# Optimization experiments

Measured on AMD Instinct MI355X. Metric: run time of the kernel, lower is better.

## Reference

```python
import jax, jax.numpy as jnp
import numpy as np

B, N, F_IN, F_OUT, H = 4, 2048, 256, 256, 4
NEG_INF = -1e9
EDGE_PROB = 0.05
LEAKY_SLOPE = 0.2  # tf.nn.leaky_relu default alpha


def setup_inputs() -> dict:
    key = jax.random.key(0)
    k_x, k_m, k_w, k_a, k_b = jax.random.split(key, 5)
    inputs = jax.random.normal(k_x, (B, N, F_IN), dtype=jnp.float32)
    # bias: additive adjacency mask, 0 on edges / -1e9 off-edges (standard GAT)
    u = jax.random.uniform(k_m, (B, N, N), dtype=jnp.float32)
    bias = jnp.where(u < EDGE_PROB, 0.0, NEG_INF).astype(jnp.float32)
    # self-loops so every softmax row has at least one valid entry
    bias = bias.at[:, jnp.arange(N), jnp.arange(N)].set(0.0)
    # per-head learned params (uniform [0,1) init as in the original)
    W = jax.random.uniform(k_w, (H, F_IN, F_OUT), dtype=jnp.float32)
    a = jax.random.uniform(k_a, (H, F_OUT), dtype=jnp.float32)
    b = jax.random.uniform(k_b, (H, F_OUT), dtype=jnp.float32)
    return {"inputs": inputs, "bias": bias, "W": W, "a": a, "b": b}


def reference(inputs, bias, W, a, b):
    # transformed: [H, B, N, F_OUT]
    t = jnp.einsum('bnf,hfo->hbno', inputs, W) + b[:, None, None, :]
    # per-node score s = t @ a : [H, B, N]
    s = jnp.einsum('hbno,ho->hbn', t, a)
    # weights[i,j] = s[i] + s[j]  (weights + transpose)
    w = s[..., :, None] + s[..., None, :]  # [H, B, N, N]
    coefs = jax.nn.softmax(jax.nn.leaky_relu(w, negative_slope=LEAKY_SLOPE) + bias, axis=-1)
    heads = jnp.einsum('hbnm,hbmo->hbno', coefs, t)  # [H, B, N, F_OUT]
    return jnp.mean(heads, axis=0)  # (1/num_heads) * add_n(heads)
```

## Files before the change

kernel.cpp:

```cpp
#include <hip/hip_runtime.h>
#include <hip/hip_bf16.h>
#include <stdint.h>

#define H 4
#define BB 4
#define NN 2048
#define FIN 256
#define FOUT 256
#define M_TOT (BB*NN)
#define LOG2E 1.44269504f

typedef float f32x4 __attribute__((ext_vector_type(4)));
typedef short s16x8 __attribute__((ext_vector_type(8)));
typedef unsigned int u32;

static __device__ __forceinline__ short f2bf(float f) {
    return __builtin_bit_cast(short, __float2bfloat16(f));
}
static __device__ __forceinline__ float bf2f(short u) {
    unsigned x = ((unsigned)(unsigned short)u) << 16;
    return __builtin_bit_cast(float, x);
}
static __device__ __forceinline__ void glds16(const void* g, void* l) {
    __builtin_amdgcn_global_load_lds(
        (const __attribute__((address_space(1))) u32*)(g),
        (__attribute__((address_space(3))) u32*)(l), 16, 0, 0);
}

__global__ __launch_bounds__(256) void k_prep(const float* __restrict__ W, const float* __restrict__ a,
                                              const float* __restrict__ bvec,
                                              short* __restrict__ WT, float* __restrict__ q,
                                              float* __restrict__ c) {
    int bid = blockIdx.x;
    if (bid < 64) {
        __shared__ float lds[64][65];
        int h = bid >> 4, kt = (bid >> 2) & 3, ot = bid & 3;
        int kb = kt * 64, ob = ot * 64;
        int tx = threadIdx.x & 63, ty = threadIdx.x >> 6;
#pragma unroll
        for (int r = 0; r < 16; ++r) {
            int k_l = ty + r * 4;
            lds[tx][k_l] = W[(size_t)(h * FIN + kb + k_l) * FOUT + ob + tx];
        }
        __syncthreads();
#pragma unroll
        for (int r = 0; r < 16; ++r) {
            int o_l = ty + r * 4;
            WT[(size_t)(h * FOUT + ob + o_l) * FIN + kb + tx] = f2bf(lds[o_l][tx]);
        }
    } else if (bid < 320) {
        int wv = ((bid - 64) * 256 + threadIdx.x) >> 6;
        int lane = threadIdx.x & 63;
        int h = wv >> 8, f = wv & 255;
        float4 w4 = *(const float4*)(W + (size_t)(h * FIN + f) * FOUT + lane * 4);
        float4 a4 = *(const float4*)(a + h * FOUT + lane * 4);
        float d = w4.x * a4.x + w4.y * a4.y + w4.z * a4.z + w4.w * a4.w;
#pragma unroll
        for (int off = 32; off; off >>= 1) d += __shfl_xor(d, off);
        if (lane == 0) q[h * FIN + f] = d;
    } else {
        int h = threadIdx.x >> 6, lane = threadIdx.x & 63;
        float4 b4 = *(const float4*)(bvec + h * FOUT + lane * 4);
        float4 a4 = *(const float4*)(a + h * FOUT + lane * 4);
        float d = b4.x * a4.x + b4.y * a4.y + b4.z * a4.z + b4.w * a4.w;
#pragma unroll
        for (int off = 32; off; off >>= 1) d += __shfl_xor(d, off);
        if (lane == 0) c[h] = d;
    }
}

__global__ __launch_bounds__(256) void k_s(const float* __restrict__ X, const float* __restrict__ q,
                                           const float* __restrict__ c, float* __restrict__ s,
                                           short* __restrict__ Xbf) {
    int m = blockIdx.x * 4 + (threadIdx.x >> 6);
    int lane = threadIdx.x & 63;
    float4 xv = *(const float4*)(X + (size_t)m * FIN + lane * 4);
    short4 xb;
    xb.x = f2bf(xv.x); xb.y = f2bf(xv.y); xb.z = f2bf(xv.z); xb.w = f2bf(xv.w);
    *(short4*)(Xbf + (size_t)m * FIN + lane * 4) = xb;
#pragma unroll
    for (int h = 0; h < H; ++h) {
        float4 qv = *(const float4*)(q + h * FIN + lane * 4);
        float d = xv.x * qv.x + xv.y * qv.y + xv.z * qv.z + xv.w * qv.w;
#pragma unroll
        for (int off = 32; off; off >>= 1) d += __shfl_xor(d, off);
        if (lane == 0) s[h * M_TOT + m] = d + c[h];
    }
}

__global__ __launch_bounds__(256) void k_maskmax(const float* __restrict__ bias, const float* __restrict__ s,
                                                 unsigned* __restrict__ mask, float* __restrict__ mx) {
    int w = threadIdx.x >> 6, lane = threadIdx.x & 63;
    int row = blockIdx.x * 4 + w;
    const float* bp = bias + (size_t)row * NN + lane * 32;
    unsigned bits = 0;
#pragma unroll
    for (int k = 0; k < 8; ++k) {
        float4 v = *(const float4*)(bp + k * 4);
        bits |= (v.x > -1.f ? 1u : 0u) << (k * 4 + 0);
        bits |= (v.y > -1.f ? 1u : 0u) << (k * 4 + 1);
        bits |= (v.z > -1.f ? 1u : 0u) << (k * 4 + 2);
        bits |= (v.w > -1.f ? 1u : 0u) << (k * 4 + 3);
    }
    mask[(size_t)row * 64 + lane] = bits;
    int b = row >> 11;
#pragma unroll
    for (int h = 0; h < H; ++h) {
        const float* sp = s + h * M_TOT + b * NN + lane * 32;
        float m = -3e38f;
#pragma unroll
        for (int k = 0; k < 8; ++k) {
            float4 sv = *(const float4*)(sp + k * 4);
            m = fmaxf(m, ((bits >> (k * 4 + 0)) & 1u) ? sv.x : -3e38f);
            m = fmaxf(m, ((bits >> (k * 4 + 1)) & 1u) ? sv.y : -3e38f);
            m = fmaxf(m, ((bits >> (k * 4 + 2)) & 1u) ? sv.z : -3e38f);
            m = fmaxf(m, ((bits >> (k * 4 + 3)) & 1u) ? sv.w : -3e38f);
        }
#pragma unroll
        for (int off = 32; off; off >>= 1) m = fmaxf(m, __shfl_xor(m, off));
        if (lane == 0) mx[h * M_TOT + row] = m;
    }
}

__global__ __launch_bounds__(256) void k_gemm_t(const short* __restrict__ WT, const short* __restrict__ Xbf,
                                                const float* __restrict__ bvec, short* __restrict__ tTs) {
    __shared__ short ot[64][136];
    int h = blockIdx.z;
    int ob = blockIdx.y * 64;
    int mb = blockIdx.x * 128;
    int tid = threadIdx.x;
    int lane = tid & 63, w = tid >> 6;
    int r16 = lane & 15, g = lane >> 4;
    int mw = mb + w * 32;
    f32x4 acc[4][2] = {};
    for (int k = 0; k < FIN; k += 32) {
        s16x8 afr[4], bfr[2];
#pragma unroll
        for (int fa = 0; fa < 4; ++fa)
            afr[fa] = *(const s16x8*)(WT + (size_t)(h * FOUT + ob + fa * 16 + r16) * FIN + k + g * 8);
#pragma unroll
        for (int fb = 0; fb < 2; ++fb)
            bfr[fb] = *(const s16x8*)(Xbf + (size_t)(mw + fb * 16 + r16) * FIN + k + g * 8);
#pragma unroll
        for (int fa = 0; fa < 4; ++fa)
#pragma unroll
            for (int fb = 0; fb < 2; ++fb)
                acc[fa][fb] = __builtin_amdgcn_mfma_f32_16x16x32_bf16(afr[fa], bfr[fb], acc[fa][fb], 0, 0, 0);
    }
#pragma unroll
    for (int fa = 0; fa < 4; ++fa) {
#pragma unroll
        for (int r = 0; r < 4; ++r) {
            int o_l = fa * 16 + g * 4 + r;
            float bv = bvec[h * FOUT + ob + o_l];
#pragma unroll
            for (int fb = 0; fb < 2; ++fb)
                ot[o_l][w * 32 + fb * 16 + r16] = f2bf(acc[fa][fb][r] + bv);
        }
    }
    __syncthreads();
    int ol0 = tid >> 4;
    int mg  = tid & 15;
    int j0  = mb + mg * 8;
    int bb  = j0 >> 11;
    int j   = j0 & 2047;
#pragma unroll
    for (int cc = 0; cc < 4; ++cc) {
        int o_l = ol0 + cc * 16;
        int o = ob + o_l;
        s16x8 v = *(const s16x8*)&ot[o_l][mg * 8];
        size_t addr = ((size_t)((h * 4 + bb) * 32 + (j >> 6))) * 16384
                    + o * 64 + ((((j >> 3) & 7) ^ (o & 7)) << 3);
        *(s16x8*)(tTs + addr) = v;
    }
}

__global__ __launch_bounds__(512, 4) void k_attn(const short* __restrict__ tTs, const float* __restrict__ s,
                                                 const unsigned* __restrict__ mask, const float* __restrict__ mx,
                                                 short* __restrict__ OT) {
    extern __shared__ short smem[];
    short* Pl = smem + 32768;

    int flat = blockIdx.x + 32 * (blockIdx.y + 4 * blockIdx.z);
    int swz = (flat & 7) * 64 + (flat >> 3);
    int qt = swz & 31, b = (swz >> 5) & 3, h = swz >> 7;
    int ib = qt * 64;

    int tid = threadIdx.x;
    int lane = tid & 63, w = tid >> 6;
    int r16 = lane & 15, g = lane >> 4;
    int par = w & 1, oh = w >> 1;
    size_t gm = (size_t)b * NN;

    const char* slab = (const char*)(tTs + (size_t)(h * 4 + b) * 32 * 16384);
    const float* srow = s + h * M_TOT + gm;

    int i = ib + oh * 16 + r16;
    float si = srow[i];
    float mxi = mx[h * M_TOT + gm + i];
    float z = si + mxi;
    float Mlog = fmaxf(z, 0.2f * z) * LOG2E;
    float siL = si * LOG2E;
    const unsigned* mk = mask + (gm + i) * 64;

    int chk = ((((par << 2) + g) ^ (r16 & 7)) << 3);
    int rdA = (oh * 64 + r16) * 64 + chk;
    int rdP = r16 * 64 + chk;
    int wrP = oh * 1024 + rdP;

    f32x4 acc[4][4] = {};
    f32x4 accl[4] = {};
    s16x8 ones;
#pragma unroll
    for (int e = 0; e < 8; ++e) ones[e] = (short)0x3F80;

    auto stage = [&](int tt, int slot) {
        const char* gs = slab + (size_t)tt * 32768 + w * 4096 + (size_t)lane * 16;
        short* ldb = smem + slot * 16384 + w * 2048;
        glds16(gs,         ldb);
        glds16(gs + 1024,  ldb + 512);
        glds16(gs + 2048,  ldb + 1024);
        glds16(gs + 3072,  ldb + 1536);
    };
    float4 psj0, psj1; unsigned pwm;
    auto preload = [&](int tt) {
        int jw = tt * 64 + par * 32;
        psj0 = *(const float4*)(srow + jw + g * 8);
        psj1 = *(const float4*)(srow + jw + g * 8 + 4);
        pwm = mk[tt * 2 + par];
    };

    stage(0, 0);
    preload(0);
    asm volatile("s_waitcnt vmcnt(0)" ::: "memory");
    __builtin_amdgcn_s_barrier();
    __builtin_amdgcn_sched_barrier(0);

    for (int t = 0; t < 32; ++t) {
        int cur = t & 1;
        if (t < 31) stage(t + 1, cur ^ 1);

        float sjv[8] = {psj0.x, psj0.y, psj0.z, psj0.w, psj1.x, psj1.y, psj1.z, psj1.w};
        unsigned bb0 = pwm >> (g * 8);
        s16x8 pb;
#pragma unroll
        for (int e = 0; e < 8; ++e) {
            float yL = fmaf(sjv[e], LOG2E, siL);
            float ly = fmaxf(yL, 0.2f * yL);
            float aa = ((bb0 >> e) & 1u) ? (ly - Mlog) : -200.f;
            pb[e] = f2bf(__builtin_amdgcn_exp2f(aa));
        }
        *(s16x8*)(Pl + wrP) = pb;

        __builtin_amdgcn_sched_barrier(0);
        asm volatile("s_waitcnt vmcnt(4) lgkmcnt(0)" ::: "memory");
        __builtin_amdgcn_s_barrier();
        __builtin_amdgcn_sched_barrier(0);

        const short* bt = smem + cur * 16384;
        s16x8 pf0 = *(const s16x8*)(Pl + 0 * 1024 + rdP);
        s16x8 pf1 = *(const s16x8*)(Pl + 1 * 1024 + rdP);
        s16x8 pf2 = *(const s16x8*)(Pl + 2 * 1024 + rdP);
        s16x8 pf3 = *(const s16x8*)(Pl + 3 * 1024 + rdP);
        __builtin_amdgcn_s_setprio(1);
#pragma unroll
        for (int f = 0; f < 4; ++f) {
            s16x8 af = *(const s16x8*)(bt + f * 1024 + rdA);
            acc[f][0] = __builtin_amdgcn_mfma_f32_16x16x32_bf16(af, pf0, acc[f][0], 0, 0, 0);
            acc[f][1] = __builtin_amdgcn_mfma_f32_16x16x32_bf16(af, pf1, acc[f][1], 0, 0, 0);
            acc[f][2] = __builtin_amdgcn_mfma_f32_16x16x32_bf16(af, pf2, acc[f][2], 0, 0, 0);
            acc[f][3] = __builtin_amdgcn_mfma_f32_16x16x32_bf16(af, pf3, acc[f][3], 0, 0, 0);
        }
        if (oh == 0) {
            accl[0] = __builtin_amdgcn_mfma_f32_16x16x32_bf16(ones, pf0, accl[0], 0, 0, 0);
            accl[1] = __builtin_amdgcn_mfma_f32_16x16x32_bf16(ones, pf1, accl[1], 0, 0, 0);
            accl[2] = __builtin_amdgcn_mfma_f32_16x16x32_bf16(ones, pf2, accl[2], 0, 0, 0);
            accl[3] = __builtin_amdgcn_mfma_f32_16x16x32_bf16(ones, pf3, accl[3], 0, 0, 0);
        }
        __builtin_amdgcn_s_setprio(0);

        if (t < 31) preload(t + 1);
        __builtin_amdgcn_sched_barrier(0);
        __builtin_amdgcn_s_barrier();
    }

    __syncthreads();
    f32x4* ex = (f32x4*)smem;
    float* pl    = (float*)Pl;
    float* plinv = (float*)Pl + 64;
    if (par) {
#pragma unroll
        for (int f = 0; f < 4; ++f)
#pragma unroll
            for (int qf = 0; qf < 4; ++qf)
                ex[(oh * 16 + f * 4 + qf) * 64 + lane] = acc[f][qf];
        if (oh == 0 && g == 0) {
#pragma unroll
            for (int qf = 0; qf < 4; ++qf) pl[qf * 16 + r16] = accl[qf][0];
        }
    }
    __syncthreads();
    if (!par && oh == 0 && g == 0) {
#pragma unroll
        for (int qf = 0; qf < 4; ++qf) {
            float ls = accl[qf][0] + pl[qf * 16 + r16];
            plinv[qf * 16 + r16] = 1.f / ls;
        }
    }
    __syncthreads();
    if (!par) {
        size_t hbase = (size_t)h * FOUT * M_TOT + gm;
#pragma unroll
        for (int f = 0; f < 4; ++f)
#pragma unroll
            for (int qf = 0; qf < 4; ++qf) {
                f32x4 v = acc[f][qf] + ex[(oh * 16 + f * 4 + qf) * 64 + lane];
                float linv = plinv[qf * 16 + r16];
                int iq = ib + qf * 16 + r16;
#pragma unroll
                for (int rr = 0; rr < 4; ++rr) {
                    int o = oh * 64 + f * 16 + g * 4 + rr;
                    OT[hbase + (size_t)o * M_TOT + iq] = f2bf(v[rr] * linv);
                }
            }
    }
}

__global__ __launch_bounds__(256) void k_reduce(const short* __restrict__ OT, float* __restrict__ out) {
    __shared__ float lds[32][72];
    int mb = blockIdx.x * 64, obt = blockIdx.y * 32;
    int tid = threadIdx.x;
    {
        int o_l = tid >> 3;
        int m_l = (tid & 7) * 8;
        float acc[8] = {};
#pragma unroll
        for (int h = 0; h < H; ++h) {
            s16x8 v = *(const s16x8*)(OT + (size_t)(h * FOUT + obt + o_l) * M_TOT + mb + m_l);
#pragma unroll
            for (int e = 0; e < 8; ++e) acc[e] += bf2f(v[e]);
        }
#pragma unroll
        for (int e = 0; e < 8; ++e) lds[o_l][m_l + e] = acc[e] * 0.25f;
    }
    __syncthreads();
    {
        int m_l = tid >> 2;
        int o_l = (tid & 3) * 8;
        float4 v0, v1;
        v0.x = lds[o_l + 0][m_l]; v0.y = lds[o_l + 1][m_l];
        v0.z = lds[o_l + 2][m_l]; v0.w = lds[o_l + 3][m_l];
        v1.x = lds[o_l + 4][m_l]; v1.y = lds[o_l + 5][m_l];
        v1.z = lds[o_l + 6][m_l]; v1.w = lds[o_l + 7][m_l];
        float* dst = out + (size_t)(mb + m_l) * FOUT + obt + o_l;
        *(float4*)dst = v0;
        *(float4*)(dst + 4) = v1;
    }
}

extern "C" void kernel_launch(void* const* d_in, const int* in_sizes, int n_in,
                              void* d_out, int out_size, void* d_ws, size_t ws_size,
                              hipStream_t stream) {
    const float* X    = (const float*)d_in[0];
    const float* bias = (const float*)d_in[1];
    const float* W    = (const float*)d_in[2];
    const float* a    = (const float*)d_in[3];
    const float* bvec = (const float*)d_in[4];
    float* out = (float*)d_out;

    char* ws = (char*)d_ws;
    short*    Xbf  = (short*)ws;
    short*    WT   = (short*)(ws + (4u << 20));
    float*    q    = (float*)(ws + (4u << 20) + (768u << 10));
    float*    c    = q + H * FIN;
    float*    s    = (float*)(ws + (5u << 20));
    float*    mxp  = (float*)(ws + (5u << 20) + (256u << 10));
    short*    tTs  = (short*)(ws + (6u << 20));
    short*    OT   = (short*)(ws + (22u << 20));
    unsigned* mask = (unsigned*)(ws + (38u << 20));

    k_prep<<<321, 256, 0, stream>>>(W, a, bvec, WT, q, c);
    k_s<<<2048, 256, 0, stream>>>(X, q, c, s, Xbf);
    k_maskmax<<<2048, 256, 0, stream>>>(bias, s, mask, mxp);
    k_gemm_t<<<dim3(64, 4, 4), 256, 0, stream>>>(WT, Xbf, bvec, tTs);
    k_attn<<<dim3(32, 4, 4), 512, 73728, stream>>>(tTs, s, mask, mxp, OT);
    k_reduce<<<dim3(128, 8), 256, 0, stream>>>(OT, out);
}
```

Before: 134.7 us.

## Load attention value fragments straight to registers in MFMA layout, drop LDS staging

k_gemm_t now writes t in a fragment-major layout so each wave in k_attn can load its MFMA A operands directly from global memory into registers, double-buffered across iterations, instead of staging tiles through LDS with global_load_lds. The row-sum is accumulated in scalar registers from the bf16 probabilities, replacing the extra ones-MFMAs, and the P buffer is double-buffered so only one barrier per iteration is needed. LDS use drops from 72KB dynamic to a small static array, and the epilogue exchange is split into two rounds to fit. k_maskmax also caches the per-batch score rows in swizzled shared memory. The cost is more vector registers for the prefetch buffers and direct global-load latency inside the loop.

```diff
diff --git a/kernel.cpp b/kernel.cpp
--- a/kernel.cpp
+++ b/kernel.cpp
@@ -20,11 +20,6 @@
 static __device__ __forceinline__ float bf2f(short u) {
     unsigned x = ((unsigned)(unsigned short)u) << 16;
     return __builtin_bit_cast(float, x);
-}
-static __device__ __forceinline__ void glds16(const void* g, void* l) {
-    __builtin_amdgcn_global_load_lds(
-        (const __attribute__((address_space(1))) u32*)(g),
-        (__attribute__((address_space(3))) u32*)(l), 16, 0, 0);
 }
 
 __global__ __launch_bounds__(256) void k_prep(const float* __restrict__ W, const float* __restrict__ a,
@@ -90,8 +85,22 @@
 
 __global__ __launch_bounds__(256) void k_maskmax(const float* __restrict__ bias, const float* __restrict__ s,
                                                  unsigned* __restrict__ mask, float* __restrict__ mx) {
-    int w = threadIdx.x >> 6, lane = threadIdx.x & 63;
-    int row = blockIdx.x * 4 + w;
+    __shared__ float sl[8192];
+    int tid = threadIdx.x;
+    int row0 = blockIdx.x * 4;
+    int b = row0 >> 11;
+#pragma unroll
+    for (int i = 0; i < 8; ++i) {
+        int flat = i * 1024 + tid * 4;
+        int h = flat >> 11, j = flat & 2047;
+        float4 v = *(const float4*)(s + (size_t)h * M_TOT + (size_t)b * NN + j);
+        int phys = flat ^ (((flat >> 5) & 7) << 2);
+        *(float4*)(sl + phys) = v;
+    }
+    __syncthreads();
+
+    int w = tid >> 6, lane = tid & 63;
+    int row = row0 + w;
     const float* bp = bias + (size_t)row * NN + lane * 32;
     unsigned bits = 0;
 #pragma unroll
@@ -103,14 +112,14 @@
         bits |= (v.w > -1.f ? 1u : 0u) << (k * 4 + 3);
     }
     mask[(size_t)row * 64 + lane] = bits;
-    int b = row >> 11;
 #pragma unroll
     for (int h = 0; h < H; ++h) {
-        const float* sp = s + h * M_TOT + b * NN + lane * 32;
         float m = -3e38f;
 #pragma unroll
         for (int k = 0; k < 8; ++k) {
-            float4 sv = *(const float4*)(sp + k * 4);
+            int flat = h * 2048 + lane * 32 + k * 4;
+            int phys = flat ^ (((flat >> 5) & 7) << 2);
+            float4 sv = *(const float4*)(sl + phys);
             m = fmaxf(m, ((bits >> (k * 4 + 0)) & 1u) ? sv.x : -3e38f);
             m = fmaxf(m, ((bits >> (k * 4 + 1)) & 1u) ? sv.y : -3e38f);
             m = fmaxf(m, ((bits >> (k * 4 + 2)) & 1u) ? sv.z : -3e38f);
@@ -159,18 +168,20 @@
         }
     }
     __syncthreads();
-    int ol0 = tid >> 4;
-    int mg  = tid & 15;
-    int j0  = mb + mg * 8;
-    int bb  = j0 >> 11;
-    int j   = j0 & 2047;
+    int bb = mb >> 11, jloc = mb & 2047;
+    int jt0 = jloc >> 6;
+    size_t slab = (size_t)((h * 4 + bb) * 32) * 16384;
 #pragma unroll
     for (int cc = 0; cc < 4; ++cc) {
-        int o_l = ol0 + cc * 16;
-        int o = ob + o_l;
-        s16x8 v = *(const s16x8*)&ot[o_l][mg * 8];
-        size_t addr = ((size_t)((h * 4 + bb) * 32 + (j >> 6))) * 16384
-                    + o * 64 + ((((j >> 3) & 7) ^ (o & 7)) << 3);
+        int sid = cc * 256 + tid;
+        int frag = sid >> 6;
+        int l = sid & 63;
+        int f_l = frag >> 2, jt_sel = (frag >> 1) & 1, par = frag & 1;
+        int o_l = f_l * 16 + (l & 15);
+        int m_l = jt_sel * 64 + par * 32 + (l >> 4) * 8;
+        s16x8 v = *(const s16x8*)&ot[o_l][m_l];
+        int fid = ((ob >> 4) + f_l) * 2 + par;
+        size_t addr = slab + (size_t)(jt0 + jt_sel) * 16384 + fid * 512 + l * 8;
         *(s16x8*)(tTs + addr) = v;
     }
 }
@@ -178,8 +189,7 @@
 __global__ __launch_bounds__(512, 4) void k_attn(const short* __restrict__ tTs, const float* __restrict__ s,
                                                  const unsigned* __restrict__ mask, const float* __restrict__ mx,
                                                  short* __restrict__ OT) {
-    extern __shared__ short smem[];
-    short* Pl = smem + 32768;
+    __shared__ short smem[16640];
 
     int flat = blockIdx.x + 32 * (blockIdx.y + 4 * blockIdx.z);
     int swz = (flat & 7) * 64 + (flat >> 3);
@@ -192,7 +202,7 @@
     int par = w & 1, oh = w >> 1;
     size_t gm = (size_t)b * NN;
 
-    const char* slab = (const char*)(tTs + (size_t)(h * 4 + b) * 32 * 16384);
+    const short* slab = tTs + (size_t)((h * 4 + b) * 32) * 16384;
     const float* srow = s + h * M_TOT + gm;
 
     int i = ib + oh * 16 + r16;
@@ -204,41 +214,32 @@
     const unsigned* mk = mask + (gm + i) * 64;
 
     int chk = ((((par << 2) + g) ^ (r16 & 7)) << 3);
-    int rdA = (oh * 64 + r16) * 64 + chk;
     int rdP = r16 * 64 + chk;
     int wrP = oh * 1024 + rdP;
 
     f32x4 acc[4][4] = {};
-    f32x4 accl[4] = {};
-    s16x8 ones;
-#pragma unroll
-    for (int e = 0; e < 8; ++e) ones[e] = (short)0x3F80;
-
-    auto stage = [&](int tt, int slot) {
-        const char* gs = slab + (size_t)tt * 32768 + w * 4096 + (size_t)lane * 16;
-        short* ldb = smem + slot * 16384 + w * 2048;
-        glds16(gs,         ldb);
-        glds16(gs + 1024,  ldb + 512);
-        glds16(gs + 2048,  ldb + 1024);
-        glds16(gs + 3072,  ldb + 1536);
-    };
+    float lsum = 0.f;
+
+    s16x8 acur[4], anext[4];
+#pragma unroll
+    for (int f = 0; f < 4; ++f)
+        acur[f] = *(const s16x8*)(slab + ((oh * 4 + f) * 2 + par) * 512 + lane * 8);
+
     float4 psj0, psj1; unsigned pwm;
-    auto preload = [&](int tt) {
-        int jw = tt * 64 + par * 32;
+    {
+        int jw = par * 32;
         psj0 = *(const float4*)(srow + jw + g * 8);
         psj1 = *(const float4*)(srow + jw + g * 8 + 4);
-        pwm = mk[tt * 2 + par];
-    };
-
-    stage(0, 0);
-    preload(0);
-    asm volatile("s_waitcnt vmcnt(0)" ::: "memory");
-    __builtin_amdgcn_s_barrier();
-    __builtin_amdgcn_sched_barrier(0);
+        pwm = mk[par];
+    }
 
     for (int t = 0; t < 32; ++t) {
-        int cur = t & 1;
-        if (t < 31) stage(t + 1, cur ^ 1);
+        if (t < 31) {
+            const short* tp = slab + (size_t)(t + 1) * 16384;
+#pragma unroll
+            for (int f = 0; f < 4; ++f)
+                anext[f] = *(const s16x8*)(tp + ((oh * 4 + f) * 2 + par) * 512 + lane * 8);
+        }
 
         float sjv[8] = {psj0.x, psj0.y, psj0.z, psj0.w, psj1.x, psj1.y, psj1.z, psj1.w};
         unsigned bb0 = pwm >> (g * 8);
@@ -248,81 +249,82 @@
             float yL = fmaf(sjv[e], LOG2E, siL);
             float ly = fmaxf(yL, 0.2f * yL);
             float aa = ((bb0 >> e) & 1u) ? (ly - Mlog) : -200.f;
-            pb[e] = f2bf(__builtin_amdgcn_exp2f(aa));
-        }
-        *(s16x8*)(Pl + wrP) = pb;
-
+            short pv = f2bf(__builtin_amdgcn_exp2f(aa));
+            pb[e] = pv;
+            lsum += bf2f(pv);
+        }
+        *(s16x8*)(smem + (t & 1) * 4096 + wrP) = pb;
+
+        if (t < 31) {
+            int jw = (t + 1) * 64 + par * 32;
+            psj0 = *(const float4*)(srow + jw + g * 8);
+            psj1 = *(const float4*)(srow + jw + g * 8 + 4);
+            pwm = mk[(t + 1) * 2 + par];
+        }
+
+        asm volatile("s_waitcnt lgkmcnt(0)" ::: "memory");
         __builtin_amdgcn_sched_barrier(0);
-        asm volatile("s_waitcnt vmcnt(4) lgkmcnt(0)" ::: "memory");
         __builtin_amdgcn_s_barrier();
         __builtin_amdgcn_sched_barrier(0);
 
-        const short* bt = smem + cur * 16384;
-        s16x8 pf0 = *(const s16x8*)(Pl + 0 * 1024 + rdP);
-        s16x8 pf1 = *(const s16x8*)(Pl + 1 * 1024 + rdP);
-        s16x8 pf2 = *(const s16x8*)(Pl + 2 * 1024 + rdP);
-        s16x8 pf3 = *(const s16x8*)(Pl + 3 * 1024 + rdP);
+        const short* Pb = smem + (t & 1) * 4096;
         __builtin_amdgcn_s_setprio(1);
 #pragma unroll
-        for (int f = 0; f < 4; ++f) {
-            s16x8 af = *(const s16x8*)(bt + f * 1024 + rdA);
-            acc[f][0] = __builtin_amdgcn_mfma_f32_16x16x32_bf16(af, pf0, acc[f][0], 0, 0, 0);
-            acc[f][1] = __builtin_amdgcn_mfma_f32_16x16x32_bf16(af, pf1, acc[f][1], 0, 0, 0);
-            acc[f][2] = __builtin_amdgcn_mfma_f32_16x16x32_bf16(af, pf2, acc[f][2], 0, 0, 0);
-            acc[f][3] = __builtin_amdgcn_mfma_f32_16x16x32_bf16(af, pf3, acc[f][3], 0, 0, 0);
-        }
-        if (oh == 0) {
-            accl[0] = __builtin_amdgcn_mfma_f32_16x16x32_bf16(ones, pf0, accl[0], 0, 0, 0);
-            accl[1] = __builtin_amdgcn_mfma_f32_16x16x32_bf16(ones, pf1, accl[1], 0, 0, 0);
-            accl[2] = __builtin_amdgcn_mfma_f32_16x16x32_bf16(ones, pf2, accl[2], 0, 0, 0);
-            accl[3] = __builtin_amdgcn_mfma_f32_16x16x32_bf16(ones, pf3, accl[3], 0, 0, 0);
+        for (int qf = 0; qf < 4; ++qf) {
+            s16x8 pf = *(const s16x8*)(Pb + qf * 1024 + rdP);
+            acc[0][qf] = __builtin_amdgcn_mfma_f32_16x16x32_bf16(acur[0], pf, acc[0][qf], 0, 0, 0);
+            acc[1][qf] = __builtin_amdgcn_mfma_f32_16x16x32_bf16(acur[1], pf, acc[1][qf], 0, 0, 0);
+            acc[2][qf] = __builtin_amdgcn_mfma_f32_16x16x32_bf16(acur[2], pf, acc[2][qf], 0, 0, 0);
+            acc[3][qf] = __builtin_amdgcn_mfma_f32_16x16x32_bf16(acur[3], pf, acc[3][qf], 0, 0, 0);
         }
         __builtin_amdgcn_s_setprio(0);
 
-        if (t < 31) preload(t + 1);
-        __builtin_amdgcn_sched_barrier(0);
-        __builtin_amdgcn_s_barrier();
-    }
-
-    __syncthreads();
+        if (t < 31) {
+#pragma unroll
+            for (int f = 0; f < 4; ++f) acur[f] = anext[f];
+        }
+    }
+
+    __syncthreads();
+    lsum += __shfl_xor(lsum, 16);
+    lsum += __shfl_xor(lsum, 32);
+    float* pl    = (float*)(smem + 16384);
+    float* plinv = pl + 64;
+    if (par == 1 && g == 0) pl[oh * 16 + r16] = lsum;
+    __syncthreads();
+    if (par == 0 && g == 0) plinv[oh * 16 + r16] = 1.f / (lsum + pl[oh * 16 + r16]);
+    __syncthreads();
+    float linv[4];
+#pragma unroll
+    for (int qf = 0; qf < 4; ++qf) linv[qf] = plinv[qf * 16 + r16];
+
     f32x4* ex = (f32x4*)smem;
-    float* pl    = (float*)Pl;
-    float* plinv = (float*)Pl + 64;
-    if (par) {
-#pragma unroll
-        for (int f = 0; f < 4; ++f)
-#pragma unroll
-            for (int qf = 0; qf < 4; ++qf)
-                ex[(oh * 16 + f * 4 + qf) * 64 + lane] = acc[f][qf];
-        if (oh == 0 && g == 0) {
-#pragma unroll
-            for (int qf = 0; qf < 4; ++qf) pl[qf * 16 + r16] = accl[qf][0];
-        }
-    }
-    __syncthreads();
-    if (!par && oh == 0 && g == 0) {
-#pragma unroll
-        for (int qf = 0; qf < 4; ++qf) {
-            float ls = accl[qf][0] + pl[qf * 16 + r16];
-            plinv[qf * 16 + r16] = 1.f / ls;
-        }
-    }
-    __syncthreads();
-    if (!par) {
-        size_t hbase = (size_t)h * FOUT * M_TOT + gm;
-#pragma unroll
-        for (int f = 0; f < 4; ++f)
-#pragma unroll
-            for (int qf = 0; qf < 4; ++qf) {
-                f32x4 v = acc[f][qf] + ex[(oh * 16 + f * 4 + qf) * 64 + lane];
-                float linv = plinv[qf * 16 + r16];
-                int iq = ib + qf * 16 + r16;
-#pragma unroll
-                for (int rr = 0; rr < 4; ++rr) {
-                    int o = oh * 64 + f * 16 + g * 4 + rr;
-                    OT[hbase + (size_t)o * M_TOT + iq] = f2bf(v[rr] * linv);
+    size_t hbase = (size_t)h * FOUT * M_TOT + gm;
+#pragma unroll
+    for (int rnd = 0; rnd < 2; ++rnd) {
+        if (par == 1 && (oh >> 1) == rnd) {
+#pragma unroll
+            for (int f = 0; f < 4; ++f)
+#pragma unroll
+                for (int qf = 0; qf < 4; ++qf)
+                    ex[(((oh & 1) * 4 + f) * 4 + qf) * 64 + lane] = acc[f][qf];
+        }
+        __syncthreads();
+        if (par == 0 && (oh >> 1) == rnd) {
+#pragma unroll
+            for (int f = 0; f < 4; ++f)
+#pragma unroll
+                for (int qf = 0; qf < 4; ++qf) {
+                    f32x4 v = acc[f][qf] + ex[(((oh & 1) * 4 + f) * 4 + qf) * 64 + lane];
+                    int iq = ib + qf * 16 + r16;
+#pragma unroll
+                    for (int rr = 0; rr < 4; ++rr) {
+                        int o = (oh * 4 + f) * 16 + g * 4 + rr;
+                        OT[hbase + (size_t)o * M_TOT + iq] = f2bf(v[rr] * linv[qf]);
+                    }
                 }
-            }
+        }
+        __syncthreads();
     }
 }
 
@@ -383,6 +385,6 @@
     k_s<<<2048, 256, 0, stream>>>(X, q, c, s, Xbf);
     k_maskmax<<<2048, 256, 0, stream>>>(bias, s, mask, mxp);
     k_gemm_t<<<dim3(64, 4, 4), 256, 0, stream>>>(WT, Xbf, bvec, tTs);
-    k_attn<<<dim3(32, 4, 4), 512, 73728, stream>>>(tTs, s, mask, mxp, OT);
+    k_attn<<<dim3(32, 4, 4), 512, 0, stream>>>(tTs, s, mask, mxp, OT);
     k_reduce<<<dim3(128, 8), 256, 0, stream>>>(OT, out);
 }
```

Measured after the change: 114.9 us. -14.7%, faster.
